# Performance work log

Measured on AMD Instinct MI355X. Metric: run time of the kernel, lower is better.

## Reference

```python
import jax, jax.numpy as jnp
import numpy as np
from jax import lax

B, S, T = 2048, 4096, 3


def setup_inputs() -> dict:
    key = jax.random.key(0)
    k_em, k_tr, k_st, k_en, k_tg = jax.random.split(key, 5)
    emissions = jax.random.normal(k_em, (B, S, T), dtype=jnp.float32)
    # reset_parameters(): uniform(-0.1, 0.1)
    transitions = jax.random.uniform(k_tr, (T, T), minval=-0.1, maxval=0.1, dtype=jnp.float32)
    start_transitions = jax.random.uniform(k_st, (T,), minval=-0.1, maxval=0.1, dtype=jnp.float32)
    end_transitions = jax.random.uniform(k_en, (T,), minval=-0.1, maxval=0.1, dtype=jnp.float32)
    tags = jax.random.randint(k_tg, (B, S), 0, T, dtype=jnp.int32)
    mask = jnp.ones((B, S), dtype=jnp.int32)
    return {
        "emissions": emissions,
        "transitions": transitions,
        "start_transitions": start_transitions,
        "end_transitions": end_transitions,
        "tags": tags,
        "mask": mask,
    }


def _crf_nll(emissions, transitions, start_transitions, end_transitions, tags, mask):
    # batch_first=True -> transpose to time-major (S, B, ...)
    em = jnp.transpose(emissions, (1, 0, 2))  # (S, B, T)
    tg = jnp.transpose(tags, (1, 0))          # (S, B)
    mk = jnp.transpose(mask, (1, 0))          # (S, B)
    batch_idx = jnp.arange(em.shape[1])

    # ---- log partition (forward algorithm) ----
    alpha0 = start_transitions[None, :] + em[0]  # (B, T)

    def fwd_step(alpha, inp):
        e, m = inp  # e: (B,T), m: (B,)
        # alpha[b,i] + trans[i,j] + e[b,j] -> logsumexp over i
        nxt = jax.nn.logsumexp(alpha[:, :, None] + transitions[None, :, :] + e[:, None, :], axis=1)
        alpha = jnp.where((m > 0)[:, None], nxt, alpha)
        return alpha, None

    alpha, _ = lax.scan(fwd_step, alpha0, (em[1:], mk[1:]))
    log_partition = jax.nn.logsumexp(alpha + end_transitions[None, :], axis=1)  # (B,)

    # ---- gold score ----
    score0 = start_transitions[tg[0]] + em[0][batch_idx, tg[0]]  # (B,)

    def score_step(carry, inp):
        score, prev = carry
        e, t, m = inp
        add = transitions[prev, t] + e[batch_idx, t]
        score = score + jnp.where(m > 0, add, jnp.zeros_like(score))
        return (score, t), None

    (score, _), _ = lax.scan(score_step, (score0, tg[0]), (em[1:], tg[1:], mk[1:]))
    seq_lens = jnp.sum(mk, axis=0)  # (B,)
    last_tags = tg[seq_lens - 1, batch_idx]
    score = score + end_transitions[last_tags]

    return jnp.mean(log_partition - score)


def reference(emissions, transitions, start_transitions, end_transitions, tags, mask):
    return _crf_nll(emissions, transitions, start_transitions, end_transitions, tags, mask)
```

## Files before the change

### kernel.cpp

```cpp
#include <hip/hip_runtime.h>
#include <math.h>

#define CRF_B 2048
#define CRF_S 4096
#define LN2F  0.6931471805599453f

#define CRF_MERGE(aq0,aq1,aq2,aq3,aq4,aq5,aq6,aq7,aq8,aC,asc,acn, \
                  bq0,bq1,bq2,bq3,bq4,bq5,bq6,bq7,bq8,bC,bsc,bcn) { \
    float r0_=aq0*bq0+aq1*bq3+aq2*bq6;                              \
    float r1_=aq0*bq1+aq1*bq4+aq2*bq7;                              \
    float r2_=aq0*bq2+aq1*bq5+aq2*bq8;                              \
    float r3_=aq3*bq0+aq4*bq3+aq5*bq6;                              \
    float r4_=aq3*bq1+aq4*bq4+aq5*bq7;                              \
    float r5_=aq3*bq2+aq4*bq5+aq5*bq8;                              \
    float r6_=aq6*bq0+aq7*bq3+aq8*bq6;                              \
    float r7_=aq6*bq1+aq7*bq4+aq8*bq7;                              \
    float r8_=aq6*bq2+aq7*bq5+aq8*bq8;                              \
    float mx_ = fmaxf(fmaxf(fmaxf(fmaxf(r0_,r1_),r2_),              \
                            fmaxf(fmaxf(r3_,r4_),r5_)),             \
                      fmaxf(fmaxf(r6_,r7_),r8_));                   \
    int ex_ = ((__float_as_int(mx_)>>23)&255)-127;                  \
    float sc_ = __int_as_float((127-ex_)<<23);                      \
    aq0=r0_*sc_; aq1=r1_*sc_; aq2=r2_*sc_;                          \
    aq3=r3_*sc_; aq4=r4_*sc_; aq5=r5_*sc_;                          \
    aq6=r6_*sc_; aq7=r7_*sc_; aq8=r8_*sc_;                          \
    aC = aC + bC + ex_;                                             \
    asc += bsc; acn += bcn; }

#define CRF_STEP(tconst, E0, E1, E2) {                               \
    int tv_ = (int)((ttag >> (2*(tconst))) & 3u);                    \
    int mv_ = (int)((tmsk >> (tconst)) & 1u);                        \
    if (mv_ && !(((tconst) == 0) && (tid == 0))) {                   \
        float X0_ = __expf(E0), X1_ = __expf(E1), X2_ = __expf(E2);  \
        float n0_, n1_, n2_;                                         \
        n0_ = q0*Etr0 + q1*Etr3 + q2*Etr6;                           \
        n1_ = q0*Etr1 + q1*Etr4 + q2*Etr7;                           \
        n2_ = q0*Etr2 + q1*Etr5 + q2*Etr8;                           \
        q0 = n0_*X0_; q1 = n1_*X1_; q2 = n2_*X2_;                    \
        n0_ = q3*Etr0 + q4*Etr3 + q5*Etr6;                           \
        n1_ = q3*Etr1 + q4*Etr4 + q5*Etr7;                           \
        n2_ = q3*Etr2 + q4*Etr5 + q5*Etr8;                           \
        q3 = n0_*X0_; q4 = n1_*X1_; q5 = n2_*X2_;                    \
        n0_ = q6*Etr0 + q7*Etr3 + q8*Etr6;                           \
        n1_ = q6*Etr1 + q7*Etr4 + q8*Etr7;                           \
        n2_ = q6*Etr2 + q7*Etr5 + q8*Etr8;                           \
        q6 = n0_*X0_; q7 = n1_*X1_; q8 = n2_*X2_;                    \
        sem += (tv_ == 0) ? (E0) : ((tv_ == 1) ? (E1) : (E2));       \
    } }

#define CRF_RENORM() {                                               \
    float mx_ = fmaxf(fmaxf(fmaxf(fmaxf(q0,q1),q2),                  \
                            fmaxf(fmaxf(q3,q4),q5)),                 \
                      fmaxf(fmaxf(q6,q7),q8));                       \
    int ex_ = ((__float_as_int(mx_) >> 23) & 255) - 127;             \
    float sc_ = __int_as_float((127 - ex_) << 23);                   \
    q0 *= sc_; q1 *= sc_; q2 *= sc_;                                 \
    q3 *= sc_; q4 *= sc_; q5 *= sc_;                                 \
    q6 *= sc_; q7 *= sc_; q8 *= sc_;                                 \
    C += ex_; }

__global__ __launch_bounds__(256, 4) void crf_row_kernel(
    const float* __restrict__ em,
    const float* __restrict__ trans,
    const float* __restrict__ startt,
    const float* __restrict__ endt,
    const int*   __restrict__ tags,
    const int*   __restrict__ mask,
    float* __restrict__ perb)
{
    __shared__ float s_tr[9];
    __shared__ float s_rq[4][10];
    __shared__ int   s_rc[4][2];

    const int tid = threadIdx.x;
    const int w = tid >> 6, l = tid & 63;
    const int b = blockIdx.x;
    const long cbase = (long)b * CRF_S + (long)tid * 16;

    if (tid < 9) s_tr[tid] = trans[tid];

    const float4* e4 = (const float4*)(em + cbase * 3);
    float4 ea0 = e4[0], ea1 = e4[1], ea2  = e4[2],  ea3  = e4[3];
    float4 ea4 = e4[4], ea5 = e4[5], ea6  = e4[6],  ea7  = e4[7];
    float4 ea8 = e4[8], ea9 = e4[9], ea10 = e4[10], ea11 = e4[11];
    const int4* t4 = (const int4*)(tags + cbase);
    const int4* m4 = (const int4*)(mask + cbase);
    int4 ta = t4[0], tb = t4[1], tc = t4[2], td = t4[3];
    int4 ma = m4[0], mb = m4[1], mc = m4[2], md = m4[3];
    int p = 0;
    if (tid > 0) p = tags[cbase - 1];

    __syncthreads();

    unsigned ttag =  (unsigned)(ta.x & 3)        | ((unsigned)(ta.y & 3) << 2)
                  | ((unsigned)(ta.z & 3) << 4)  | ((unsigned)(ta.w & 3) << 6)
                  | ((unsigned)(tb.x & 3) << 8)  | ((unsigned)(tb.y & 3) << 10)
                  | ((unsigned)(tb.z & 3) << 12) | ((unsigned)(tb.w & 3) << 14)
                  | ((unsigned)(tc.x & 3) << 16) | ((unsigned)(tc.y & 3) << 18)
                  | ((unsigned)(tc.z & 3) << 20) | ((unsigned)(tc.w & 3) << 22)
                  | ((unsigned)(td.x & 3) << 24) | ((unsigned)(td.y & 3) << 26)
                  | ((unsigned)(td.z & 3) << 28) | ((unsigned)(td.w & 3) << 30);
    unsigned tmsk =  (unsigned)(ma.x != 0)        | ((unsigned)(ma.y != 0) << 1)
                  | ((unsigned)(ma.z != 0) << 2)  | ((unsigned)(ma.w != 0) << 3)
                  | ((unsigned)(mb.x != 0) << 4)  | ((unsigned)(mb.y != 0) << 5)
                  | ((unsigned)(mb.z != 0) << 6)  | ((unsigned)(mb.w != 0) << 7)
                  | ((unsigned)(mc.x != 0) << 8)  | ((unsigned)(mc.y != 0) << 9)
                  | ((unsigned)(mc.z != 0) << 10) | ((unsigned)(mc.w != 0) << 11)
                  | ((unsigned)(md.x != 0) << 12) | ((unsigned)(md.y != 0) << 13)
                  | ((unsigned)(md.z != 0) << 14) | ((unsigned)(md.w != 0) << 15);

    float str_sum = 0.f;
    {
        int pr = p;
        #pragma unroll
        for (int t = 0; t < 16; ++t) {
            int tv = (int)((ttag >> (2 * t)) & 3u);
            if (((tmsk >> t) & 1u) && !((t == 0) && (tid == 0)))
                str_sum += s_tr[pr * 3 + tv];
            pr = tv;
        }
    }
    int cnt = __popc(tmsk & ((tid == 0) ? 0xFFFEu : 0xFFFFu));

    float Etr0 = __expf(s_tr[0]), Etr1 = __expf(s_tr[1]), Etr2 = __expf(s_tr[2]);
    float Etr3 = __expf(s_tr[3]), Etr4 = __expf(s_tr[4]), Etr5 = __expf(s_tr[5]);
    float Etr6 = __expf(s_tr[6]), Etr7 = __expf(s_tr[7]), Etr8 = __expf(s_tr[8]);

    float q0=1.f,q1=0.f,q2=0.f, q3=0.f,q4=1.f,q5=0.f, q6=0.f,q7=0.f,q8=1.f;
    int C = 0;
    float sem = 0.f;

    float et0 = ea0.x, et1 = ea0.y, et2 = ea0.z;

    CRF_STEP( 0, ea0.x, ea0.y, ea0.z);
    CRF_STEP( 1, ea0.w, ea1.x, ea1.y);
    CRF_STEP( 2, ea1.z, ea1.w, ea2.x);
    CRF_STEP( 3, ea2.y, ea2.z, ea2.w);
    CRF_RENORM();
    CRF_STEP( 4, ea3.x, ea3.y, ea3.z);
    CRF_STEP( 5, ea3.w, ea4.x, ea4.y);
    CRF_STEP( 6, ea4.z, ea4.w, ea5.x);
    CRF_STEP( 7, ea5.y, ea5.z, ea5.w);
    CRF_RENORM();
    CRF_STEP( 8, ea6.x, ea6.y, ea6.z);
    CRF_STEP( 9, ea6.w, ea7.x, ea7.y);
    CRF_STEP(10, ea7.z, ea7.w, ea8.x);
    CRF_STEP(11, ea8.y, ea8.z, ea8.w);
    CRF_RENORM();
    CRF_STEP(12, ea9.x, ea9.y, ea9.z);
    CRF_STEP(13, ea9.w, ea10.x, ea10.y);
    CRF_STEP(14, ea10.z, ea10.w, ea11.x);
    CRF_STEP(15, ea11.y, ea11.z, ea11.w);
    CRF_RENORM();

    float score = str_sum + sem;

    #pragma unroll
    for (int st = 1; st < 64; st <<= 1) {
        float nq0 = __shfl_down(q0, st), nq1 = __shfl_down(q1, st),
              nq2 = __shfl_down(q2, st), nq3 = __shfl_down(q3, st),
              nq4 = __shfl_down(q4, st), nq5 = __shfl_down(q5, st),
              nq6 = __shfl_down(q6, st), nq7 = __shfl_down(q7, st),
              nq8 = __shfl_down(q8, st);
        int   nC  = __shfl_down(C, st);
        float nsc = __shfl_down(score, st);
        int   ncn = __shfl_down(cnt, st);
        CRF_MERGE(q0,q1,q2,q3,q4,q5,q6,q7,q8,C,score,cnt,
                  nq0,nq1,nq2,nq3,nq4,nq5,nq6,nq7,nq8,nC,nsc,ncn);
    }

    if (l == 0) {
        s_rq[w][0]=q0; s_rq[w][1]=q1; s_rq[w][2]=q2;
        s_rq[w][3]=q3; s_rq[w][4]=q4; s_rq[w][5]=q5;
        s_rq[w][6]=q6; s_rq[w][7]=q7; s_rq[w][8]=q8;
        s_rq[w][9]=score;
        s_rc[w][0]=C;  s_rc[w][1]=cnt;
    }
    __syncthreads();

    if (tid == 0) {
        float a0=q0, a1=q1, a2=q2, a3=q3, a4=q4, a5=q5, a6=q6, a7=q7, a8=q8;
        float asc = score;
        int AC = C, acn = cnt;
        #pragma unroll
        for (int w2 = 1; w2 < 4; ++w2) {
            float m0=s_rq[w2][0], m1=s_rq[w2][1], m2=s_rq[w2][2],
                  m3=s_rq[w2][3], m4=s_rq[w2][4], m5=s_rq[w2][5],
                  m6=s_rq[w2][6], m7=s_rq[w2][7], m8=s_rq[w2][8];
            float msc = s_rq[w2][9];
            int mC = s_rc[w2][0], mcn = s_rc[w2][1];
            CRF_MERGE(a0,a1,a2,a3,a4,a5,a6,a7,a8,AC,asc,acn,
                      m0,m1,m2,m3,m4,m5,m6,m7,m8,mC,msc,mcn);
        }
        int tg0 = (int)(ttag & 3u), mk0 = (int)(tmsk & 1u);
        float la0 = startt[0] + et0;
        float la1 = startt[1] + et1;
        float la2 = startt[2] + et2;
        float am = fmaxf(fmaxf(la0, la1), la2);
        float w0  = __expf(la0 - am);
        float w1  = __expf(la1 - am);
        float w2v = __expf(la2 - am);
        float v0 = w0*a0 + w1*a3 + w2v*a6;
        float v1 = w0*a1 + w1*a4 + w2v*a7;
        float v2 = w0*a2 + w1*a5 + w2v*a8;
        float sum = v0 * __expf(endt[0]) + v1 * __expf(endt[1])
                  + v2 * __expf(endt[2]);
        float lp = am + (float)AC * LN2F + __logf(sum);

        float sc = asc + startt[tg0]
                 + ((tg0 == 0) ? et0 : (tg0 == 1) ? et1 : et2);
        int cn = acn + mk0;
        int lastidx = (cn > 0) ? (cn - 1) : 0;
        sc += endt[tags[(long)b * CRF_S + lastidx]];

        perb[b] = lp - sc;
    }
}

__global__ __launch_bounds__(256) void crf_reduce_kernel(
    const float* __restrict__ perb, float* __restrict__ out)
{
    __shared__ float sdata[256];
    const int tid = threadIdx.x;
    float s = 0.f;
    for (int i = tid; i < CRF_B; i += 256) s += perb[i];
    sdata[tid] = s;
    __syncthreads();
    for (int off = 128; off > 0; off >>= 1) {
        if (tid < off) sdata[tid] += sdata[tid + off];
        __syncthreads();
    }
    if (tid == 0) out[0] = sdata[0] * (1.0f / (float)CRF_B);
}

extern "C" void kernel_launch(void* const* d_in, const int* in_sizes, int n_in,
                              void* d_out, int out_size, void* d_ws, size_t ws_size,
                              hipStream_t stream)
{
    const float* em     = (const float*)d_in[0];
    const float* trans  = (const float*)d_in[1];
    const float* startt = (const float*)d_in[2];
    const float* endt   = (const float*)d_in[3];
    const int*   tags   = (const int*)d_in[4];
    const int*   mask   = (const int*)d_in[5];
    float* out = (float*)d_out;

    float* perb = (float*)d_ws;

    crf_row_kernel<<<CRF_B, 256, 0, stream>>>(
        em, trans, startt, endt, tags, mask, perb);
    crf_reduce_kernel<<<1, 256, 0, stream>>>(perb, out);
}
```

Measured before the change: 38.51 us.

## Split CRF row kernel into sync-free chunk pass and single-block combine pass

The row kernel no longer uses shared memory or __syncthreads. Transitions are read straight from global memory. The previous tag now comes from a warp shuffle, and the gold transition sum is built from a packed 5-bit histogram of transition pairs. Each wave writes its partial transfer matrix to workspace, and a single 1024-thread block merges the four wave partials per row, adds the start and end terms and reduces to the mean. The intent is to remove block barriers and the serial tid-0 tail from the main kernel and to raise occupancy, at the cost of workspace traffic and a serial single-block combine.

```diff
diff --git a/kernel.cpp b/kernel.cpp
--- a/kernel.cpp
+++ b/kernel.cpp
@@ -46,7 +46,9 @@
         n2_ = q6*Etr2 + q7*Etr5 + q8*Etr8;                           \
         q6 = n0_*X0_; q7 = n1_*X1_; q8 = n2_*X2_;                    \
         sem += (tv_ == 0) ? (E0) : ((tv_ == 1) ? (E1) : (E2));       \
-    } }
+        hist += 1ULL << (5 * (p * 3 + tv_));                         \
+    }                                                                \
+    p = tv_; }
 
 #define CRF_RENORM() {                                               \
     float mx_ = fmaxf(fmaxf(fmaxf(fmaxf(q0,q1),q2),                  \
@@ -59,25 +61,17 @@
     q6 *= sc_; q7 *= sc_; q8 *= sc_;                                 \
     C += ex_; }
 
-__global__ __launch_bounds__(256, 4) void crf_row_kernel(
+__global__ __launch_bounds__(256, 6) void crf_chunkA(
     const float* __restrict__ em,
     const float* __restrict__ trans,
-    const float* __restrict__ startt,
-    const float* __restrict__ endt,
     const int*   __restrict__ tags,
     const int*   __restrict__ mask,
-    float* __restrict__ perb)
+    float* __restrict__ wsq)
 {
-    __shared__ float s_tr[9];
-    __shared__ float s_rq[4][10];
-    __shared__ int   s_rc[4][2];
-
     const int tid = threadIdx.x;
     const int w = tid >> 6, l = tid & 63;
     const int b = blockIdx.x;
     const long cbase = (long)b * CRF_S + (long)tid * 16;
-
-    if (tid < 9) s_tr[tid] = trans[tid];
 
     const float4* e4 = (const float4*)(em + cbase * 3);
     float4 ea0 = e4[0], ea1 = e4[1], ea2  = e4[2],  ea3  = e4[3];
@@ -87,10 +81,12 @@
     const int4* m4 = (const int4*)(mask + cbase);
     int4 ta = t4[0], tb = t4[1], tc = t4[2], td = t4[3];
     int4 ma = m4[0], mb = m4[1], mc = m4[2], md = m4[3];
-    int p = 0;
-    if (tid > 0) p = tags[cbase - 1];
-
-    __syncthreads();
+    int pload = 0;
+    if (l == 0 && tid > 0) pload = tags[cbase - 1];
+
+    float Etr0 = __expf(trans[0]), Etr1 = __expf(trans[1]), Etr2 = __expf(trans[2]);
+    float Etr3 = __expf(trans[3]), Etr4 = __expf(trans[4]), Etr5 = __expf(trans[5]);
+    float Etr6 = __expf(trans[6]), Etr7 = __expf(trans[7]), Etr8 = __expf(trans[8]);
 
     unsigned ttag =  (unsigned)(ta.x & 3)        | ((unsigned)(ta.y & 3) << 2)
                   | ((unsigned)(ta.z & 3) << 4)  | ((unsigned)(ta.w & 3) << 6)
@@ -109,28 +105,16 @@
                   | ((unsigned)(md.x != 0) << 12) | ((unsigned)(md.y != 0) << 13)
                   | ((unsigned)(md.z != 0) << 14) | ((unsigned)(md.w != 0) << 15);
 
-    float str_sum = 0.f;
-    {
-        int pr = p;
-        #pragma unroll
-        for (int t = 0; t < 16; ++t) {
-            int tv = (int)((ttag >> (2 * t)) & 3u);
-            if (((tmsk >> t) & 1u) && !((t == 0) && (tid == 0)))
-                str_sum += s_tr[pr * 3 + tv];
-            pr = tv;
-        }
-    }
+    int lastTag = (int)((ttag >> 30) & 3u);
+    int pup = __shfl_up(lastTag, 1);
+    int p = (l == 0) ? (pload & 3) : pup;
+
     int cnt = __popc(tmsk & ((tid == 0) ? 0xFFFEu : 0xFFFFu));
-
-    float Etr0 = __expf(s_tr[0]), Etr1 = __expf(s_tr[1]), Etr2 = __expf(s_tr[2]);
-    float Etr3 = __expf(s_tr[3]), Etr4 = __expf(s_tr[4]), Etr5 = __expf(s_tr[5]);
-    float Etr6 = __expf(s_tr[6]), Etr7 = __expf(s_tr[7]), Etr8 = __expf(s_tr[8]);
 
     float q0=1.f,q1=0.f,q2=0.f, q3=0.f,q4=1.f,q5=0.f, q6=0.f,q7=0.f,q8=1.f;
     int C = 0;
     float sem = 0.f;
-
-    float et0 = ea0.x, et1 = ea0.y, et2 = ea0.z;
+    unsigned long long hist = 0ULL;
 
     CRF_STEP( 0, ea0.x, ea0.y, ea0.z);
     CRF_STEP( 1, ea0.w, ea1.x, ea1.y);
@@ -153,6 +137,10 @@
     CRF_STEP(15, ea11.y, ea11.z, ea11.w);
     CRF_RENORM();
 
+    float str_sum = 0.f;
+    #pragma unroll
+    for (int i2 = 0; i2 < 9; ++i2)
+        str_sum += (float)(int)((hist >> (5 * i2)) & 31ULL) * trans[i2];
     float score = str_sum + sem;
 
     #pragma unroll
@@ -170,63 +158,76 @@
     }
 
     if (l == 0) {
-        s_rq[w][0]=q0; s_rq[w][1]=q1; s_rq[w][2]=q2;
-        s_rq[w][3]=q3; s_rq[w][4]=q4; s_rq[w][5]=q5;
-        s_rq[w][6]=q6; s_rq[w][7]=q7; s_rq[w][8]=q8;
-        s_rq[w][9]=score;
-        s_rc[w][0]=C;  s_rc[w][1]=cnt;
-    }
-    __syncthreads();
-
-    if (tid == 0) {
-        float a0=q0, a1=q1, a2=q2, a3=q3, a4=q4, a5=q5, a6=q6, a7=q7, a8=q8;
-        float asc = score;
-        int AC = C, acn = cnt;
+        float4* o = (float4*)(wsq + ((size_t)b * 4 + w) * 12);
+        o[0] = make_float4(q0, q1, q2, q3);
+        o[1] = make_float4(q4, q5, q6, q7);
+        o[2] = make_float4(q8, score, __int_as_float(C), __int_as_float(cnt));
+    }
+}
+
+__global__ __launch_bounds__(1024) void crf_combineB(
+    const float* __restrict__ em,
+    const float* __restrict__ startt,
+    const float* __restrict__ endt,
+    const int*   __restrict__ tags,
+    const int*   __restrict__ mask,
+    const float* __restrict__ wsq,
+    float* __restrict__ out)
+{
+    __shared__ float sdata[1024];
+    const int tid = threadIdx.x;
+    float local = 0.f;
+
+    #pragma unroll
+    for (int rr = 0; rr < 2; ++rr) {
+        const int row = tid + rr * 1024;
+        const float4* pb = (const float4*)(wsq + (size_t)row * 4 * 12);
+        float4 a0 = pb[0], a1 = pb[1], a2 = pb[2];
+        float q0=a0.x,q1=a0.y,q2=a0.z,q3=a0.w,q4=a1.x,q5=a1.y,q6=a1.z,q7=a1.w,
+              q8=a2.x;
+        float score = a2.y;
+        int C = __float_as_int(a2.z), cnt = __float_as_int(a2.w);
         #pragma unroll
         for (int w2 = 1; w2 < 4; ++w2) {
-            float m0=s_rq[w2][0], m1=s_rq[w2][1], m2=s_rq[w2][2],
-                  m3=s_rq[w2][3], m4=s_rq[w2][4], m5=s_rq[w2][5],
-                  m6=s_rq[w2][6], m7=s_rq[w2][7], m8=s_rq[w2][8];
-            float msc = s_rq[w2][9];
-            int mC = s_rc[w2][0], mcn = s_rc[w2][1];
-            CRF_MERGE(a0,a1,a2,a3,a4,a5,a6,a7,a8,AC,asc,acn,
+            float4 b0 = pb[3*w2+0], b1 = pb[3*w2+1], b2 = pb[3*w2+2];
+            float m0=b0.x,m1=b0.y,m2=b0.z,m3=b0.w,m4=b1.x,m5=b1.y,m6=b1.z,
+                  m7=b1.w,m8=b2.x;
+            float msc = b2.y;
+            int mC = __float_as_int(b2.z), mcn = __float_as_int(b2.w);
+            CRF_MERGE(q0,q1,q2,q3,q4,q5,q6,q7,q8,C,score,cnt,
                       m0,m1,m2,m3,m4,m5,m6,m7,m8,mC,msc,mcn);
         }
-        int tg0 = (int)(ttag & 3u), mk0 = (int)(tmsk & 1u);
-        float la0 = startt[0] + et0;
-        float la1 = startt[1] + et1;
-        float la2 = startt[2] + et2;
+        const long base = (long)row * CRF_S;
+        float e0 = em[base*3+0], e1 = em[base*3+1], e2 = em[base*3+2];
+        int tg0 = tags[base] & 3;
+        int mk0 = (mask[base] != 0) ? 1 : 0;
+
+        float la0 = startt[0] + e0;
+        float la1 = startt[1] + e1;
+        float la2 = startt[2] + e2;
         float am = fmaxf(fmaxf(la0, la1), la2);
         float w0  = __expf(la0 - am);
         float w1  = __expf(la1 - am);
         float w2v = __expf(la2 - am);
-        float v0 = w0*a0 + w1*a3 + w2v*a6;
-        float v1 = w0*a1 + w1*a4 + w2v*a7;
-        float v2 = w0*a2 + w1*a5 + w2v*a8;
+        float v0 = w0*q0 + w1*q3 + w2v*q6;
+        float v1 = w0*q1 + w1*q4 + w2v*q7;
+        float v2 = w0*q2 + w1*q5 + w2v*q8;
         float sum = v0 * __expf(endt[0]) + v1 * __expf(endt[1])
                   + v2 * __expf(endt[2]);
-        float lp = am + (float)AC * LN2F + __logf(sum);
-
-        float sc = asc + startt[tg0]
-                 + ((tg0 == 0) ? et0 : (tg0 == 1) ? et1 : et2);
-        int cn = acn + mk0;
+        float lp = am + (float)C * LN2F + __logf(sum);
+
+        float sc = score + startt[tg0]
+                 + ((tg0 == 0) ? e0 : (tg0 == 1) ? e1 : e2);
+        int cn = cnt + mk0;
         int lastidx = (cn > 0) ? (cn - 1) : 0;
-        sc += endt[tags[(long)b * CRF_S + lastidx]];
-
-        perb[b] = lp - sc;
-    }
-}
-
-__global__ __launch_bounds__(256) void crf_reduce_kernel(
-    const float* __restrict__ perb, float* __restrict__ out)
-{
-    __shared__ float sdata[256];
-    const int tid = threadIdx.x;
-    float s = 0.f;
-    for (int i = tid; i < CRF_B; i += 256) s += perb[i];
-    sdata[tid] = s;
+        sc += endt[tags[base + lastidx]];
+
+        local += lp - sc;
+    }
+
+    sdata[tid] = local;
     __syncthreads();
-    for (int off = 128; off > 0; off >>= 1) {
+    for (int off = 512; off > 0; off >>= 1) {
         if (tid < off) sdata[tid] += sdata[tid + off];
         __syncthreads();
     }
@@ -245,9 +246,8 @@
     const int*   mask   = (const int*)d_in[5];
     float* out = (float*)d_out;
 
-    float* perb = (float*)d_ws;
-
-    crf_row_kernel<<<CRF_B, 256, 0, stream>>>(
-        em, trans, startt, endt, tags, mask, perb);
-    crf_reduce_kernel<<<1, 256, 0, stream>>>(perb, out);
+    float* wsq = (float*)d_ws;
+
+    crf_chunkA<<<CRF_B, 256, 0, stream>>>(em, trans, tags, mask, wsq);
+    crf_combineB<<<1, 1024, 0, stream>>>(em, startt, endt, tags, mask, wsq, out);
 }
```

Result: slower. 95.51 us (+148.0%).
